# Optimization experiments

Measured on AMD Instinct MI355X. Metric: run time of the kernel, lower is better.

## Reference

```python
import jax, jax.numpy as jnp
import numpy as np


def _apply_ry(state, angle, wire):
    # state: (B, P, 2,2,2,2) real statevector; angle: scalar or (B, P)
    ax = 2 + wire
    st = jnp.moveaxis(state, ax, -1)
    c = jnp.cos(angle * 0.5)
    s = jnp.sin(angle * 0.5)
    extra = st.ndim - 1 - jnp.ndim(c)
    c = jnp.reshape(c, jnp.shape(c) + (1,) * extra)
    s = jnp.reshape(s, jnp.shape(s) + (1,) * extra)
    s0, s1 = st[..., 0], st[..., 1]
    out = jnp.stack([c * s0 - s * s1, s * s0 + c * s1], axis=-1)
    return jnp.moveaxis(out, -1, ax)


def _apply_cnot(state, control, target):
    st = jnp.moveaxis(state, (2 + control, 2 + target), (-2, -1))
    out = jnp.stack([st[..., 0, :], st[..., 1, ::-1]], axis=-2)
    return jnp.moveaxis(out, (-2, -1), (2 + control, 2 + target))


def _run_circuit(patch_vals, params):
    # patch_vals: (B, P, 4) angles; params: (L, 4). All gates (RY, CNOT) are real,
    # so the statevector stays real float32. Simulates all B*P circuits at once.
    B, P, _ = patch_vals.shape
    state = jnp.zeros((B, P, 2, 2, 2, 2), patch_vals.dtype).at[:, :, 0, 0, 0, 0].set(1.0)
    for w in range(4):
        state = _apply_ry(state, patch_vals[:, :, w], w)
    for l in range(params.shape[0]):
        state = _apply_ry(state, params[l, 0], 0)
        state = _apply_ry(state, params[l, 1], 1)
        state = _apply_cnot(state, 0, 1)
        state = _apply_ry(state, params[l, 2], 2)
        state = _apply_ry(state, params[l, 3], 3)
        state = _apply_cnot(state, 2, 3)
    prob = state * state
    # <Z_w> = P(bit_w = 0) - P(bit_w = 1)
    z = [(jnp.take(prob, 0, axis=2 + w) - jnp.take(prob, 1, axis=2 + w)).sum(axis=(2, 3, 4))
         for w in range(4)]
    return jnp.stack(z, axis=-1)  # (B, P, 4)


def _forward(x, params, W, b):
    B = x.shape[0]
    xi = x[:, 0]  # (B, 28, 28)
    # torch Unfold(2, stride=2): per-patch order (kh, kw); patches row-major -> (B, 196, 4)
    p2 = xi.reshape(B, 14, 2, 14, 2).transpose(0, 1, 3, 2, 4).reshape(B, 196, 4)
    qfeat = _run_circuit(p2, params).reshape(B, 196 * 4)  # (B, 784), patch-major
    # torch Unfold(4, stride=4) gives (B, 16, 49); .view(B, -1) -> (kernel_pos, patch) order
    cfeat = xi.reshape(B, 7, 4, 7, 4).transpose(0, 2, 4, 1, 3).reshape(B, 16 * 49)
    feats = jnp.concatenate([qfeat, cfeat], axis=1)  # (B, 1568)
    logits = feats @ W.T + b
    return jax.nn.log_softmax(logits, axis=-1)


def setup_inputs():
    key = jax.random.key(0)
    k1, k2, k3 = jax.random.split(key, 3)
    B = 2048
    x = jax.random.normal(k1, (B, 1, 28, 28), dtype=jnp.float32)
    params = jax.random.normal(k2, (4, 4), dtype=jnp.float32)
    W = jax.random.normal(k3, (10, 1568), dtype=jnp.float32) * 0.05
    b = jnp.zeros((10,), dtype=jnp.float32)
    return {"x": x, "params": params, "W": W, "b": b}


def reference(x, params, W, b):
    return _forward(x, params, W, b)
```

## Files before the change

kernel.cpp:

```cpp
#include <hip/hip_runtime.h>
#include <math.h>

#define TPB 512

typedef __fp16 half2v __attribute__((ext_vector_type(2)));
typedef __fp16 half4v __attribute__((ext_vector_type(4)));
typedef __fp16 half8v __attribute__((ext_vector_type(8)));

template <int CTRL, int RMASK>
__device__ inline float dpp_add(float v) {
    int t = __builtin_amdgcn_update_dpp(0, __float_as_int(v), CTRL, RMASK, 0xf, false);
    return v + __int_as_float(t);
}
__device__ inline float wave_sum_bcast(float v) {
    v = dpp_add<0x111, 0xf>(v);
    v = dpp_add<0x112, 0xf>(v);
    v = dpp_add<0x114, 0xf>(v);
    v = dpp_add<0x118, 0xf>(v);
    v = dpp_add<0x142, 0xa>(v);
    v = dpp_add<0x143, 0xc>(v);
    return __int_as_float(__builtin_amdgcn_readlane(__float_as_int(v), 63));
}

#if __has_builtin(__builtin_amdgcn_fdot2)
#define HAVE_FDOT2 1
#else
#define HAVE_FDOT2 0
#endif

__global__ __launch_bounds__(TPB) void quanv_one_kernel(
    const float* __restrict__ x,
    const float* __restrict__ params,
    const float* __restrict__ W,
    const float* __restrict__ bias,
    float* __restrict__ out,
    int B, int L)
{
    __shared__ __align__(16) __fp16 wlds[15680];
    __shared__ __align__(16) float umat[32];

    const int tid  = threadIdx.x;
    const int lane = tid & 63;
    const int wv   = tid >> 6;

    for (int g = tid; g < 3920; g += TPB) {
        int flat = g * 4;
        int c  = flat / 1568;
        int r  = flat - c * 1568;
        int t  = r >> 3;
        int kh = r & 7;
        half4v o;
        if (kh == 0) {
            float4 q = *(const float4*)(W + c * 1568 + t * 4);
            o[0] = (__fp16)q.x; o[1] = (__fp16)q.y;
            o[2] = (__fp16)q.z; o[3] = (__fp16)q.w;
        } else {
#pragma unroll
            for (int k = 0; k < 4; ++k) {
                int p = t * 4 + k;
                int row = p / 28, col = p - row * 28;
                int gf = (((row & 3) * 4 + (col & 3)) * 7 + (row >> 2)) * 7 + (col >> 2);
                o[k] = (__fp16)W[c * 1568 + 784 + gf];
            }
        }
        *(half4v*)(wlds + flat) = o;
    }

    if (tid < 2) {
        const int f = tid;
        float M[16];
#pragma unroll
        for (int i = 0; i < 16; ++i) M[i] = (i % 5 == 0) ? 1.f : 0.f;
        for (int l = 0; l < L; ++l) {
            float A = params[4 * l + 2 * f + 0] * 0.5f;
            float C = __cosf(A), S = __sinf(A);
#pragma unroll
            for (int q = 0; q < 4; ++q) {
                float a0 = M[q],     a2 = M[8 + q];
                M[q]      = C * a0 - S * a2;  M[8 + q]  = S * a0 + C * a2;
                float a1 = M[4 + q], a3 = M[12 + q];
                M[4 + q]  = C * a1 - S * a3;  M[12 + q] = S * a1 + C * a3;
            }
            A = params[4 * l + 2 * f + 1] * 0.5f;
            C = __cosf(A); S = __sinf(A);
#pragma unroll
            for (int q = 0; q < 4; ++q) {
                float a0 = M[q],     a1 = M[4 + q];
                M[q]      = C * a0 - S * a1;  M[4 + q]  = S * a0 + C * a1;
                float a2 = M[8 + q], a3 = M[12 + q];
                M[8 + q]  = C * a2 - S * a3;  M[12 + q] = S * a2 + C * a3;
            }
#pragma unroll
            for (int q = 0; q < 4; ++q) {
                float tm = M[8 + q]; M[8 + q] = M[12 + q]; M[12 + q] = tm;
            }
        }
#pragma unroll
        for (int i = 0; i < 16; ++i) umat[f * 16 + i] = M[i];
    }

    __syncthreads();

    const int img = blockIdx.x * 8 + wv;
    if (img >= B) return;

    float Um[32];
#pragma unroll
    for (int j = 0; j < 8; ++j) ((float4*)Um)[j] = ((const float4*)umat)[j];

    const float* xb = x + (size_t)img * 784;

    float acc[10];
#pragma unroll
    for (int c = 0; c < 10; ++c) acc[c] = 0.f;

#pragma unroll
    for (int r = 0; r < 4; ++r) {
        int t = r * 64 + lane;
        if (t < 196) {
            int pi = t / 14, pj = t - pi * 14;
            float2 top = *(const float2*)(xb + 56 * pi + 2 * pj);
            float2 bot = *(const float2*)(xb + 56 * pi + 2 * pj + 28);
            float4 cim = *(const float4*)(xb + 4 * t);

            float c0 = __cosf(0.5f * top.x), s0 = __sinf(0.5f * top.x);
            float c1 = __cosf(0.5f * top.y), s1 = __sinf(0.5f * top.y);
            float c2 = __cosf(0.5f * bot.x), s2 = __sinf(0.5f * bot.x);
            float c3 = __cosf(0.5f * bot.y), s3 = __sinf(0.5f * bot.y);

            float ui0 = c0 * c1, ui1 = c0 * s1, ui2 = s0 * c1, ui3 = s0 * s1;
            float vi0 = c2 * c3, vi1 = c2 * s3, vi2 = s2 * c3, vi3 = s2 * s3;

            float uf0 = fmaf(Um[0],  ui0, fmaf(Um[1],  ui1, fmaf(Um[2],  ui2, Um[3]  * ui3)));
            float uf1 = fmaf(Um[4],  ui0, fmaf(Um[5],  ui1, fmaf(Um[6],  ui2, Um[7]  * ui3)));
            float uf2 = fmaf(Um[8],  ui0, fmaf(Um[9],  ui1, fmaf(Um[10], ui2, Um[11] * ui3)));
            float uf3 = fmaf(Um[12], ui0, fmaf(Um[13], ui1, fmaf(Um[14], ui2, Um[15] * ui3)));
            float vf0 = fmaf(Um[16], vi0, fmaf(Um[17], vi1, fmaf(Um[18], vi2, Um[19] * vi3)));
            float vf1 = fmaf(Um[20], vi0, fmaf(Um[21], vi1, fmaf(Um[22], vi2, Um[23] * vi3)));
            float vf2 = fmaf(Um[24], vi0, fmaf(Um[25], vi1, fmaf(Um[26], vi2, Um[27] * vi3)));
            float vf3 = fmaf(Um[28], vi0, fmaf(Um[29], vi1, fmaf(Um[30], vi2, Um[31] * vi3)));

            float p0 = uf0 * uf0, p1 = uf1 * uf1, p2 = uf2 * uf2, p3 = uf3 * uf3;
            float q0 = vf0 * vf0, q1 = vf1 * vf1, q2 = vf2 * vf2, q3 = vf3 * vf3;
            float z0 = (p0 + p1) - (p2 + p3);
            float z1 = (p0 + p2) - (p1 + p3);
            float z2 = (q0 + q1) - (q2 + q3);
            float z3 = (q0 + q2) - (q1 + q3);

            half2v f0 = __builtin_amdgcn_cvt_pkrtz(z0, z1);
            half2v f1 = __builtin_amdgcn_cvt_pkrtz(z2, z3);
            half2v f2 = __builtin_amdgcn_cvt_pkrtz(cim.x, cim.y);
            half2v f3 = __builtin_amdgcn_cvt_pkrtz(cim.z, cim.w);

#pragma unroll
            for (int c = 0; c < 10; ++c) {
                half8v w = *(const half8v*)(wlds + (c * 196 + t) * 8);
                half2v w0 = __builtin_shufflevector(w, w, 0, 1);
                half2v w1 = __builtin_shufflevector(w, w, 2, 3);
                half2v w2 = __builtin_shufflevector(w, w, 4, 5);
                half2v w3 = __builtin_shufflevector(w, w, 6, 7);
                float a = acc[c];
#if HAVE_FDOT2
                a = __builtin_amdgcn_fdot2(f0, w0, a, false);
                a = __builtin_amdgcn_fdot2(f1, w1, a, false);
                a = __builtin_amdgcn_fdot2(f2, w2, a, false);
                a = __builtin_amdgcn_fdot2(f3, w3, a, false);
#else
                a = fmaf((float)f0[0], (float)w0[0], a);
                a = fmaf((float)f0[1], (float)w0[1], a);
                a = fmaf((float)f1[0], (float)w1[0], a);
                a = fmaf((float)f1[1], (float)w1[1], a);
                a = fmaf((float)f2[0], (float)w2[0], a);
                a = fmaf((float)f2[1], (float)w2[1], a);
                a = fmaf((float)f3[0], (float)w3[0], a);
                a = fmaf((float)f3[1], (float)w3[1], a);
#endif
                acc[c] = a;
            }
        }
    }

    float l0 = wave_sum_bcast(acc[0]) + bias[0];
    float l1 = wave_sum_bcast(acc[1]) + bias[1];
    float l2 = wave_sum_bcast(acc[2]) + bias[2];
    float l3 = wave_sum_bcast(acc[3]) + bias[3];
    float l4 = wave_sum_bcast(acc[4]) + bias[4];
    float l5 = wave_sum_bcast(acc[5]) + bias[5];
    float l6 = wave_sum_bcast(acc[6]) + bias[6];
    float l7 = wave_sum_bcast(acc[7]) + bias[7];
    float l8 = wave_sum_bcast(acc[8]) + bias[8];
    float l9 = wave_sum_bcast(acc[9]) + bias[9];

    float m = fmaxf(fmaxf(fmaxf(fmaxf(l0, l1), fmaxf(l2, l3)),
                          fmaxf(fmaxf(l4, l5), fmaxf(l6, l7))),
                    fmaxf(l8, l9));
    float se = __expf(l0 - m) + __expf(l1 - m) + __expf(l2 - m) + __expf(l3 - m) +
               __expf(l4 - m) + __expf(l5 - m) + __expf(l6 - m) + __expf(l7 - m) +
               __expf(l8 - m) + __expf(l9 - m);
    float lse = __logf(se) + m;

    if (lane < 10) {
        float o = l0 - lse;
        o = (lane == 1) ? l1 - lse : o;
        o = (lane == 2) ? l2 - lse : o;
        o = (lane == 3) ? l3 - lse : o;
        o = (lane == 4) ? l4 - lse : o;
        o = (lane == 5) ? l5 - lse : o;
        o = (lane == 6) ? l6 - lse : o;
        o = (lane == 7) ? l7 - lse : o;
        o = (lane == 8) ? l8 - lse : o;
        o = (lane == 9) ? l9 - lse : o;
        out[(size_t)img * 10 + lane] = o;
    }
}

extern "C" void kernel_launch(void* const* d_in, const int* in_sizes, int n_in,
                              void* d_out, int out_size, void* d_ws, size_t ws_size,
                              hipStream_t stream) {
    const float* x      = (const float*)d_in[0];
    const float* params = (const float*)d_in[1];
    const float* W      = (const float*)d_in[2];
    const float* bias   = (const float*)d_in[3];
    float* out          = (float*)d_out;

    const int B = in_sizes[0] / 784;
    const int L = in_sizes[1] / 4;

    const int nblk = (B + 7) / 8;
    quanv_one_kernel<<<dim3(nblk), dim3(TPB), 0, stream>>>(x, params, W, bias, out, B, L);
}
```

Measured before the change: 14.37 us.

## Split each image across two waves and combine partial logits through LDS

Each image is now processed by two waves, each covering 98 of the 196 patches. Their partial logit sums are combined through a small shared-memory buffer before one wave does the log-softmax. This doubles the grid to 512 blocks so more CUs have work, and it shortens each wave's serial loop from 4 iterations to 2. The cost is that the fp16 W staging into LDS, which every block does, now happens twice as often in total, plus an extra block barrier; launch bounds are also raised to request 4 blocks per CU.

```diff
diff --git a/kernel.cpp b/kernel.cpp
--- a/kernel.cpp
+++ b/kernel.cpp
@@ -28,7 +28,7 @@
 #define HAVE_FDOT2 0
 #endif
 
-__global__ __launch_bounds__(TPB) void quanv_one_kernel(
+__global__ __launch_bounds__(TPB, 4) void quanv_one_kernel(
     const float* __restrict__ x,
     const float* __restrict__ params,
     const float* __restrict__ W,
@@ -38,6 +38,7 @@
 {
     __shared__ __align__(16) __fp16 wlds[15680];
     __shared__ __align__(16) float umat[32];
+    __shared__ float red[8][10];
 
     const int tid  = threadIdx.x;
     const int lane = tid & 63;
@@ -101,8 +102,9 @@
 
     __syncthreads();
 
-    const int img = blockIdx.x * 8 + wv;
-    if (img >= B) return;
+    const int imgIdx = blockIdx.x * 4 + (wv >> 1);
+    const int half   = wv & 1;
+    const int img    = (imgIdx < B) ? imgIdx : (B - 1);
 
     float Um[32];
 #pragma unroll
@@ -114,10 +116,11 @@
 #pragma unroll
     for (int c = 0; c < 10; ++c) acc[c] = 0.f;
 
-#pragma unroll
-    for (int r = 0; r < 4; ++r) {
-        int t = r * 64 + lane;
-        if (t < 196) {
+    const int tlim = 98 * (half + 1);
+#pragma unroll
+    for (int r = 0; r < 2; ++r) {
+        int t = 98 * half + r * 64 + lane;
+        if (t < tlim) {
             int pi = t / 14, pj = t - pi * 14;
             float2 top = *(const float2*)(xb + 56 * pi + 2 * pj);
             float2 bot = *(const float2*)(xb + 56 * pi + 2 * pj + 28);
@@ -180,37 +183,55 @@
         }
     }
 
-    float l0 = wave_sum_bcast(acc[0]) + bias[0];
-    float l1 = wave_sum_bcast(acc[1]) + bias[1];
-    float l2 = wave_sum_bcast(acc[2]) + bias[2];
-    float l3 = wave_sum_bcast(acc[3]) + bias[3];
-    float l4 = wave_sum_bcast(acc[4]) + bias[4];
-    float l5 = wave_sum_bcast(acc[5]) + bias[5];
-    float l6 = wave_sum_bcast(acc[6]) + bias[6];
-    float l7 = wave_sum_bcast(acc[7]) + bias[7];
-    float l8 = wave_sum_bcast(acc[8]) + bias[8];
-    float l9 = wave_sum_bcast(acc[9]) + bias[9];
-
-    float m = fmaxf(fmaxf(fmaxf(fmaxf(l0, l1), fmaxf(l2, l3)),
-                          fmaxf(fmaxf(l4, l5), fmaxf(l6, l7))),
-                    fmaxf(l8, l9));
-    float se = __expf(l0 - m) + __expf(l1 - m) + __expf(l2 - m) + __expf(l3 - m) +
-               __expf(l4 - m) + __expf(l5 - m) + __expf(l6 - m) + __expf(l7 - m) +
-               __expf(l8 - m) + __expf(l9 - m);
-    float lse = __logf(se) + m;
-
+    float s0 = wave_sum_bcast(acc[0]);
+    float s1 = wave_sum_bcast(acc[1]);
+    float s2 = wave_sum_bcast(acc[2]);
+    float s3 = wave_sum_bcast(acc[3]);
+    float s4 = wave_sum_bcast(acc[4]);
+    float s5 = wave_sum_bcast(acc[5]);
+    float s6 = wave_sum_bcast(acc[6]);
+    float s7 = wave_sum_bcast(acc[7]);
+    float s8 = wave_sum_bcast(acc[8]);
+    float s9 = wave_sum_bcast(acc[9]);
     if (lane < 10) {
-        float o = l0 - lse;
-        o = (lane == 1) ? l1 - lse : o;
-        o = (lane == 2) ? l2 - lse : o;
-        o = (lane == 3) ? l3 - lse : o;
-        o = (lane == 4) ? l4 - lse : o;
-        o = (lane == 5) ? l5 - lse : o;
-        o = (lane == 6) ? l6 - lse : o;
-        o = (lane == 7) ? l7 - lse : o;
-        o = (lane == 8) ? l8 - lse : o;
-        o = (lane == 9) ? l9 - lse : o;
-        out[(size_t)img * 10 + lane] = o;
+        float o = s0;
+        o = (lane == 1) ? s1 : o;
+        o = (lane == 2) ? s2 : o;
+        o = (lane == 3) ? s3 : o;
+        o = (lane == 4) ? s4 : o;
+        o = (lane == 5) ? s5 : o;
+        o = (lane == 6) ? s6 : o;
+        o = (lane == 7) ? s7 : o;
+        o = (lane == 8) ? s8 : o;
+        o = (lane == 9) ? s9 : o;
+        red[wv][lane] = o;
+    }
+    __syncthreads();
+
+    if (half == 0 && imgIdx < B) {
+        float lg[10];
+#pragma unroll
+        for (int c = 0; c < 10; ++c) lg[c] = red[wv][c] + red[wv + 1][c] + bias[c];
+        float m = lg[0];
+#pragma unroll
+        for (int c = 1; c < 10; ++c) m = fmaxf(m, lg[c]);
+        float se = 0.f;
+#pragma unroll
+        for (int c = 0; c < 10; ++c) se += __expf(lg[c] - m);
+        float lse = __logf(se) + m;
+        if (lane < 10) {
+            float o = lg[0];
+            o = (lane == 1) ? lg[1] : o;
+            o = (lane == 2) ? lg[2] : o;
+            o = (lane == 3) ? lg[3] : o;
+            o = (lane == 4) ? lg[4] : o;
+            o = (lane == 5) ? lg[5] : o;
+            o = (lane == 6) ? lg[6] : o;
+            o = (lane == 7) ? lg[7] : o;
+            o = (lane == 8) ? lg[8] : o;
+            o = (lane == 9) ? lg[9] : o;
+            out[(size_t)imgIdx * 10 + lane] = o - lse;
+        }
     }
 }
 
@@ -226,6 +247,6 @@
     const int B = in_sizes[0] / 784;
     const int L = in_sizes[1] / 4;
 
-    const int nblk = (B + 7) / 8;
+    const int nblk = (B + 3) / 4;
     quanv_one_kernel<<<dim3(nblk), dim3(TPB), 0, stream>>>(x, params, W, bias, out, B, L);
 }
```

Measured after the change: 16.74 us. 1.17x slower.
